# Optimization experiments

Hardware: AMD Instinct MI355X
Metric: run time of the kernel (lower is better)

The kernel has to match this reference:

```python
import jax, jax.numpy as jnp
import numpy as np

T = 2048
HID = 4096
H = 32
HKV = 8
D = 128
EPS = 1e-5
THETA = 1e6
WINDOW = 1024


def setup_inputs() -> dict:
    key = jax.random.key(0)
    k1, k2, k3 = jax.random.split(key, 3)
    return {
        "positions": jnp.arange(T, dtype=jnp.int32),
        "hidden_states": jax.random.normal(k1, (T, HID), dtype=jnp.float32),
        "w_qkv": jax.random.normal(k2, (HID, (H + 2 * HKV) * D), dtype=jnp.float32) * 0.02,
        "q_norm_w": jnp.ones((D,), dtype=jnp.float32),
        "k_norm_w": jnp.ones((D,), dtype=jnp.float32),
        "w_o": jax.random.normal(k3, (H * D, HID), dtype=jnp.float32) * 0.02,
    }


def _rmsnorm(x, w):
    # per-head RMSNorm over last dim (head_dim)
    var = jnp.mean(x * x, axis=-1, keepdims=True)
    return x * jax.lax.rsqrt(var + EPS) * w


def _rope_neox(x, positions):
    # x: [T, heads, D]; neox style: rotate halves
    half = D // 2
    inv_freq = 1.0 / (THETA ** (jnp.arange(0, half, dtype=jnp.float32) / half))
    ang = positions.astype(jnp.float32)[:, None] * inv_freq  # [T, half]
    cos = jnp.cos(ang)[:, None, :]
    sin = jnp.sin(ang)[:, None, :]
    x1, x2 = x[..., :half], x[..., half:]
    return jnp.concatenate([x1 * cos - x2 * sin, x2 * cos + x1 * sin], axis=-1)


def reference(positions, hidden_states, w_qkv, q_norm_w, k_norm_w, w_o):
    qkv = hidden_states @ w_qkv  # [T, (H+2Hkv)*D]
    q, k, v = jnp.split(qkv, [H * D, (H + HKV) * D], axis=-1)
    q = _rmsnorm(q.reshape(T, H, D), q_norm_w)
    k = _rmsnorm(k.reshape(T, HKV, D), k_norm_w)
    v = v.reshape(T, HKV, D)

    q = _rope_neox(q, positions)
    k = _rope_neox(k, positions)

    # GQA: expand kv heads to H
    rep = H // HKV
    k = jnp.repeat(k, rep, axis=1)  # [T, H, D]
    v = jnp.repeat(v, rep, axis=1)

    scale = D ** -0.5
    scores = jnp.einsum('thd,shd->hts', q, k) * scale  # [H, T, T]
    i = jnp.arange(T)[:, None]
    j = jnp.arange(T)[None, :]
    mask = (j <= i) & (i - j < WINDOW)  # causal + sliding window
    scores = jnp.where(mask[None], scores, -jnp.inf)
    probs = jax.nn.softmax(scores, axis=-1)
    attn = jnp.einsum('hts,shd->thd', probs, v).reshape(T, H * D)
    return attn @ w_o
```

## Files before the change

### kernel.cpp

```cpp
#include <hip/hip_runtime.h>
#include <hip/hip_bf16.h>
#include <stdint.h>

#define T_SEQ  2048
#define HIDDEN 4096
#define NHEAD  32
#define NKV    8
#define HDIM   128
#define NQKV   6144
#define WINDOW 1024
#define SCALE  0.08838834764831845f
#define SHIFT  12.0f

typedef __attribute__((ext_vector_type(8))) short          short8;
typedef __attribute__((ext_vector_type(8))) unsigned short ushort8_t;
typedef __attribute__((ext_vector_type(4))) float          floatx4;

__device__ __forceinline__ unsigned short f2bf(float f) {
    union { float f; unsigned int u; } v; v.f = f;
    unsigned int u = v.u;
    unsigned int r = (u + 0x7FFFu + ((u >> 16) & 1u)) >> 16;
    return (unsigned short)r;
}
__device__ __forceinline__ float bf2f(unsigned short u) {
    union { unsigned int u; float f; } v; v.u = ((unsigned int)u) << 16;
    return v.f;
}

#define GLOBAL_AS(p) ((const __attribute__((address_space(1))) void*)(p))
#define LDS_AS(p)    ((__attribute__((address_space(3))) void*)(p))

#define S_BARRIER() do { asm volatile("" ::: "memory");  \
                         __builtin_amdgcn_s_barrier();   \
                         asm volatile("" ::: "memory"); } while (0)

__global__ __launch_bounds__(256) void convert_bf16_kernel(
        const float* __restrict__ X, unsigned short* __restrict__ Y, int n4) {
    int i = blockIdx.x * blockDim.x + threadIdx.x;
    if (i < n4) {
        float4 v = ((const float4*)X)[i];
        ushort4 o;
        o.x = f2bf(v.x); o.y = f2bf(v.y); o.z = f2bf(v.z); o.w = f2bf(v.w);
        ((ushort4*)Y)[i] = o;
    }
}

__global__ __launch_bounds__(256) void transpose_bf16_kernel(
        const float* __restrict__ W, unsigned short* __restrict__ Wt, int K, int N) {
    __shared__ float tile[128][33];
    const int n0 = blockIdx.x * 32, k0 = blockIdx.y * 128;
    const int tid = threadIdx.x;
    const int rr = tid >> 3, cc = tid & 7;
    #pragma unroll
    for (int p = 0; p < 4; ++p) {
        int r = p * 32 + rr;
        float4 v = *(const float4*)&W[(size_t)(k0 + r) * N + n0 + cc * 4];
        tile[r][cc * 4 + 0] = v.x; tile[r][cc * 4 + 1] = v.y;
        tile[r][cc * 4 + 2] = v.z; tile[r][cc * 4 + 3] = v.w;
    }
    __syncthreads();
    const int nL = tid >> 3, kc = tid & 7;
    #pragma unroll
    for (int q = 0; q < 2; ++q) {
        int kbase = kc * 8 + q * 64;
        ushort8_t o;
        #pragma unroll
        for (int j = 0; j < 8; ++j) o[j] = f2bf(tile[kbase + j][nL]);
        *(ushort8_t*)&Wt[(size_t)(n0 + nL) * K + k0 + kbase] = o;
    }
}

#define STG3_A(bufi, kt, r)                                                       \
    __builtin_amdgcn_global_load_lds(                                             \
        GLOBAL_AS(A + (size_t)(m0 + rRow[r]) * K + ((kt) << 6) + rOff[r]),        \
        LDS_AS(&As3[bufi][((r) * 256 + tid) * 8]), 16, 0, 0)
#define STG3_B(bufi, kt, r)                                                       \
    __builtin_amdgcn_global_load_lds(                                             \
        GLOBAL_AS(B + (size_t)(n0 + rRow[r]) * K + ((kt) << 6) + rOff[r]),        \
        LDS_AS(&Bs3[bufi][((r) * 256 + tid) * 8]), 16, 0, 0)

template <bool BF16_OUT>
__global__ __launch_bounds__(256, 2) void gemm_bt3_kernel(
        const unsigned short* __restrict__ A,
        const unsigned short* __restrict__ B,
        void* __restrict__ Cv, int M, int N, int K) {
    __shared__ __align__(16) unsigned short As3[2][128 * 64];
    __shared__ __align__(16) unsigned short Bs3[2][128 * 64];

    const int tid  = threadIdx.x;
    const int lane = tid & 63, wave = tid >> 6;
    const int wr = wave >> 1, wc = wave & 1;
    const int lrow = lane & 15, hi = lane >> 4;

    const int nwg = gridDim.x * gridDim.y;
    int wg = blockIdx.y * gridDim.x + blockIdx.x;
    wg = (wg & 7) * (nwg >> 3) + (wg >> 3);
    const int bx = wg % gridDim.x;
    const int by = wg / gridDim.x;
    const int m0 = by * 128, n0 = bx * 128;

    const int NT = K >> 6;

    int rRow[4], rOff[4];
    #pragma unroll
    for (int r = 0; r < 4; ++r) {
        int idx = r * 256 + tid;
        int row = idx >> 3;
        rRow[r] = row;
        rOff[r] = ((idx & 7) ^ (row & 7)) * 8;
    }

    const int sA0   = (hi ^ (lrow & 7)) * 8;
    const int aBase = (wr * 64 + lrow) * 64;
    const int bBase = (wc * 64 + lrow) * 64;

    floatx4 acc[4][4] = {};

    auto kstep = [&](int cur, int t2, int mode) {
        const unsigned short* ap = &As3[cur][0];
        const unsigned short* bp = &Bs3[cur][0];
        short8 af[4][2], bf[4][2];
        #pragma unroll
        for (int m = 0; m < 4; ++m)
            #pragma unroll
            for (int kh = 0; kh < 2; ++kh)
                af[m][kh] = *(const short8*)(ap + aBase + m * 1024 + (sA0 ^ (kh << 5)));
        #pragma unroll
        for (int n = 0; n < 4; ++n)
            #pragma unroll
            for (int kh = 0; kh < 2; ++kh)
                bf[n][kh] = *(const short8*)(bp + bBase + n * 1024 + (sA0 ^ (kh << 5)));
        asm volatile("s_waitcnt lgkmcnt(0)" ::: "memory");
        __builtin_amdgcn_s_barrier();
        asm volatile("" ::: "memory");
        if (mode == 0) {
            #pragma unroll
            for (int r = 0; r < 4; ++r) STG3_A(cur, t2, r);
            #pragma unroll
            for (int r = 0; r < 4; ++r) STG3_B(cur, t2, r);
        }
        __builtin_amdgcn_s_setprio(1);
        #pragma unroll
        for (int m = 0; m < 4; ++m)
            #pragma unroll
            for (int n = 0; n < 4; ++n) {
                acc[m][n] = __builtin_amdgcn_mfma_f32_16x16x32_bf16(
                    af[m][0], bf[n][0], acc[m][n], 0, 0, 0);
                acc[m][n] = __builtin_amdgcn_mfma_f32_16x16x32_bf16(
                    af[m][1], bf[n][1], acc[m][n], 0, 0, 0);
            }
        __builtin_amdgcn_s_setprio(0);
        if (mode == 0) {
            asm volatile("s_waitcnt vmcnt(8)" ::: "memory");
            __builtin_amdgcn_s_barrier();
            asm volatile("" ::: "memory");
        } else if (mode == 1) {
            asm volatile("s_waitcnt vmcnt(0)" ::: "memory");
            __builtin_amdgcn_s_barrier();
            asm volatile("" ::: "memory");
        }
    };

    #pragma unroll
    for (int r = 0; r < 4; ++r) STG3_A(0, 0, r);
    #pragma unroll
    for (int r = 0; r < 4; ++r) STG3_B(0, 0, r);
    #pragma unroll
    for (int r = 0; r < 4; ++r) STG3_A(1, 1, r);
    #pragma unroll
    for (int r = 0; r < 4; ++r) STG3_B(1, 1, r);
    asm volatile("s_waitcnt vmcnt(8)" ::: "memory");
    S_BARRIER();

    int t = 0;
    for (; t < NT - 2; ++t) kstep(t & 1, t + 2, 0);
    kstep(t & 1, 0, 1); ++t;
    kstep(t & 1, 0, 2);

    const int rowb = hi * 4, col = lrow;
    #pragma unroll
    for (int mi = 0; mi < 4; ++mi)
        #pragma unroll
        for (int ni = 0; ni < 4; ++ni) {
            size_t base = (size_t)(m0 + wr * 64 + mi * 16 + rowb) * N
                        + (n0 + wc * 64 + ni * 16 + col);
            #pragma unroll
            for (int r = 0; r < 4; ++r) {
                if (BF16_OUT)
                    ((unsigned short*)Cv)[base + (size_t)r * N] = f2bf(acc[mi][ni][r]);
                else
                    ((float*)Cv)[base + (size_t)r * N] = acc[mi][ni][r];
            }
        }
}

#define STG4_A(bufi, kt, r)                                                       \
    __builtin_amdgcn_global_load_lds(                                             \
        GLOBAL_AS(A + (size_t)(m0 + rRowA[r]) * K + ((kt) << 6) + rOffA[r]),      \
        LDS_AS(&As4[bufi][((r) * 256 + tid) * 8]), 16, 0, 0)
#define STG4_B(bufi, kt, r)                                                       \
    __builtin_amdgcn_global_load_lds(                                             \
        GLOBAL_AS(B + (size_t)(n0 + rRowB[r]) * K + ((kt) << 6) + rOffB[r]),      \
        LDS_AS(&Bs4[bufi][((r) * 256 + tid) * 8]), 16, 0, 0)

template <bool BF16_OUT>
__global__ __launch_bounds__(256, 2) void gemm_bt4_kernel(
        const unsigned short* __restrict__ A,
        const unsigned short* __restrict__ B,
        void* __restrict__ Cv, int M, int N, int K) {
    __shared__ __align__(16) unsigned short As4[2][128 * 64];
    __shared__ __align__(16) unsigned short Bs4[2][192 * 64];

    const int tid  = threadIdx.x;
    const int lane = tid & 63, wave = tid >> 6;
    const int wr = wave >> 1, wc = wave & 1;
    const int lrow = lane & 15, hi = lane >> 4;

    const int nwg = gridDim.x * gridDim.y;
    int wg = blockIdx.y * gridDim.x + blockIdx.x;
    wg = (wg & 7) * (nwg >> 3) + (wg >> 3);
    const int by = wg % gridDim.x;
    const int bx = wg / gridDim.x;
    const int m0 = by * 128, n0 = bx * 192;

    const int NT = K >> 6;

    int rRowA[4], rOffA[4];
    #pragma unroll
    for (int r = 0; r < 4; ++r) {
        int idx = r * 256 + tid;
        int row = idx >> 3;
        rRowA[r] = row;
        rOffA[r] = ((idx & 7) ^ (row & 7)) * 8;
    }
    int rRowB[6], rOffB[6];
    #pragma unroll
    for (int r = 0; r < 6; ++r) {
        int idx = r * 256 + tid;
        int row = idx >> 3;
        rRowB[r] = row;
        rOffB[r] = ((idx & 7) ^ (row & 7)) * 8;
    }

    const int sA0   = (hi ^ (lrow & 7)) * 8;
    const int aBase = (wr * 64 + lrow) * 64;
    const int bBase = (wc * 96 + lrow) * 64;

    floatx4 acc[4][6] = {};

    auto kstep = [&](int cur, int t2, int mode) {
        const unsigned short* ap = &As4[cur][0];
        const unsigned short* bp = &Bs4[cur][0];
        short8 af[4][2], bf[6][2];
        #pragma unroll
        for (int m = 0; m < 4; ++m)
            #pragma unroll
            for (int kh = 0; kh < 2; ++kh)
                af[m][kh] = *(const short8*)(ap + aBase + m * 1024 + (sA0 ^ (kh << 5)));
        #pragma unroll
        for (int n = 0; n < 6; ++n)
            #pragma unroll
            for (int kh = 0; kh < 2; ++kh)
                bf[n][kh] = *(const short8*)(bp + bBase + n * 1024 + (sA0 ^ (kh << 5)));
        asm volatile("s_waitcnt lgkmcnt(0)" ::: "memory");
        __builtin_amdgcn_s_barrier();
        asm volatile("" ::: "memory");
        if (mode == 0) {
            #pragma unroll
            for (int r = 0; r < 4; ++r) STG4_A(cur, t2, r);
            #pragma unroll
            for (int r = 0; r < 6; ++r) STG4_B(cur, t2, r);
        }
        __builtin_amdgcn_s_setprio(1);
        #pragma unroll
        for (int m = 0; m < 4; ++m)
            #pragma unroll
            for (int n = 0; n < 6; ++n) {
                acc[m][n] = __builtin_amdgcn_mfma_f32_16x16x32_bf16(
                    af[m][0], bf[n][0], acc[m][n], 0, 0, 0);
                acc[m][n] = __builtin_amdgcn_mfma_f32_16x16x32_bf16(
                    af[m][1], bf[n][1], acc[m][n], 0, 0, 0);
            }
        __builtin_amdgcn_s_setprio(0);
        if (mode == 0) {
            asm volatile("s_waitcnt vmcnt(10)" ::: "memory");
            __builtin_amdgcn_s_barrier();
            asm volatile("" ::: "memory");
        } else if (mode == 1) {
            asm volatile("s_waitcnt vmcnt(0)" ::: "memory");
            __builtin_amdgcn_s_barrier();
            asm volatile("" ::: "memory");
        }
    };

    #pragma unroll
    for (int r = 0; r < 4; ++r) STG4_A(0, 0, r);
    #pragma unroll
    for (int r = 0; r < 6; ++r) STG4_B(0, 0, r);
    #pragma unroll
    for (int r = 0; r < 4; ++r) STG4_A(1, 1, r);
    #pragma unroll
    for (int r = 0; r < 6; ++r) STG4_B(1, 1, r);
    asm volatile("s_waitcnt vmcnt(10)" ::: "memory");
    S_BARRIER();

    int t = 0;
    for (; t < NT - 2; ++t) kstep(t & 1, t + 2, 0);
    kstep(t & 1, 0, 1); ++t;
    kstep(t & 1, 0, 2);

    const int rowb = hi * 4, col = lrow;
    #pragma unroll
    for (int mi = 0; mi < 4; ++mi)
        #pragma unroll
        for (int ni = 0; ni < 6; ++ni) {
            size_t base = (size_t)(m0 + wr * 64 + mi * 16 + rowb) * N
                        + (n0 + wc * 96 + ni * 16 + col);
            #pragma unroll
            for (int r = 0; r < 4; ++r) {
                if (BF16_OUT)
                    ((unsigned short*)Cv)[base + (size_t)r * N] = f2bf(acc[mi][ni][r]);
                else
                    ((float*)Cv)[base + (size_t)r * N] = acc[mi][ni][r];
            }
        }
}

__global__ __launch_bounds__(256) void rope_table_kernel(
        const int* __restrict__ positions, float2* __restrict__ rope) {
    int idx = blockIdx.x * 256 + threadIdx.x;
    int t = idx >> 6, i = idx & 63;
    float inv_freq = expf((float)i * -0.2158673524681918f);
    float sn, cs;
    sincosf((float)positions[t] * inv_freq, &sn, &cs);
    rope[idx] = make_float2(cs, sn);
}

__global__ __launch_bounds__(256) void qkv_post_kernel(
        const unsigned short* __restrict__ qkv, const float2* __restrict__ rope,
        const float* __restrict__ qw, const float* __restrict__ kw,
        unsigned short* __restrict__ qb,
        unsigned short* __restrict__ kb,
        unsigned short* __restrict__ vbT) {
    const int head = blockIdx.y;
    const int t0   = blockIdx.x * 32;
    const int tid  = threadIdx.x;

    if (head < 40) {
        const int r  = tid >> 3;
        const int q8 = tid & 7;
        const int t  = t0 + r;
        const unsigned short* src = qkv + (size_t)t * NQKV
                         + (head < 32 ? head * 128 : 4096 + (head - 32) * 128)
                         + q8 * 16;
        const float* w = (head < 32) ? qw : kw;

        ushort8_t u0 = *(const ushort8_t*)src;
        ushort8_t u1 = *(const ushort8_t*)(src + 8);
        float x[16];
        #pragma unroll
        for (int j = 0; j < 8; ++j) { x[j] = bf2f(u0[j]); x[8 + j] = bf2f(u1[j]); }

        float ss = 0.f;
        #pragma unroll
        for (int j = 0; j < 16; ++j) ss = fmaf(x[j], x[j], ss);
        ss += __shfl_xor(ss, 1); ss += __shfl_xor(ss, 2); ss += __shfl_xor(ss, 4);
        float sc = rsqrtf(ss * (1.f / 128.f) + 1e-5f);

        float xn[16], xp[16];
        #pragma unroll
        for (int j = 0; j < 16; ++j) xn[j] = x[j] * sc * w[q8 * 16 + j];
        #pragma unroll
        for (int j = 0; j < 16; ++j) xp[j] = __shfl_xor(xn[j], 4);

        const float2* rp = rope + (size_t)t * 64 + (q8 & 3) * 16;
        ushort8_t o0, o1;
        #pragma unroll
        for (int j = 0; j < 8; ++j) {
            float2 cs = rp[j];
            float res = (q8 < 4) ? (xn[j] * cs.x - xp[j] * cs.y)
                                 : (xn[j] * cs.x + xp[j] * cs.y);
            o0[j] = f2bf(res);
        }
        #pragma unroll
        for (int j = 0; j < 8; ++j) {
            float2 cs = rp[8 + j];
            float res = (q8 < 4) ? (xn[8+j] * cs.x - xp[8+j] * cs.y)
                                 : (xn[8+j] * cs.x + xp[8+j] * cs.y);
            o1[j] = f2bf(res);
        }
        unsigned short* dst = (head < 32)
            ? qb + ((size_t)t * 32 + head) * 128 + q8 * 16
            : kb + ((size_t)t * 8 + (head - 32)) * 128 + q8 * 16;
        *(ushort8_t*)dst       = o0;
        *(ushort8_t*)(dst + 8) = o1;
    } else {
        __shared__ float tile[128][33];
        const int hk = head - 40;
        {
            const int r = tid >> 3, c8 = tid & 7;
            const unsigned short* src =
                qkv + (size_t)(t0 + r) * NQKV + 5120 + hk * 128 + c8 * 16;
            ushort8_t u0 = *(const ushort8_t*)src;
            ushort8_t u1 = *(const ushort8_t*)(src + 8);
            #pragma unroll
            for (int j = 0; j < 8; ++j) {
                tile[c8 * 16 + j][r]     = bf2f(u0[j]);
                tile[c8 * 16 + 8 + j][r] = bf2f(u1[j]);
            }
        }
        __syncthreads();
        {
            const int d = tid >> 1, th = tid & 1;
            ushort8_t o0, o1;
            #pragma unroll
            for (int j = 0; j < 8; ++j) o0[j] = f2bf(tile[d][th * 16 + j]);
            #pragma unroll
            for (int j = 0; j < 8; ++j) o1[j] = f2bf(tile[d][th * 16 + 8 + j]);
            unsigned short* dst = vbT + ((size_t)hk * 128 + d) * T_SEQ + t0 + th * 16;
            *(ushort8_t*)dst       = o0;
            *(ushort8_t*)(dst + 8) = o1;
        }
    }
}

__global__ __launch_bounds__(256) void attention_kernel(
        const unsigned short* __restrict__ qb,
        const unsigned short* __restrict__ kb,
        const unsigned short* __restrict__ vbT,
        unsigned short* __restrict__ attnb) {
    const int h    = blockIdx.x & 31;
    const int Q0   = (blockIdx.x >> 5) * 64;
    const int tid  = threadIdx.x, wave = tid >> 6, lane = tid & 63;
    const int keyA = lane & 15, g = lane >> 4;
    const int hk   = h >> 2;
    const int qlo  = Q0 + wave * 16;

    __shared__ __align__(16) unsigned short ks [2][32 * 128];
    __shared__ __align__(16) unsigned short vsT[2][128 * 32];
    __shared__ __align__(16) unsigned short Pa [4 * 16 * 40];

    unsigned short* pw = Pa + wave * 640;

    int kRow[2], kOff[2], vD[2], vOff[2];
    #pragma unroll
    for (int i = 0; i < 2; ++i) {
        int c = i * 256 + tid;
        {   int row = c >> 4, u = c & 15;
            kRow[i] = row; kOff[i] = (u ^ (row & 7)) * 8; }
        {   int d = c >> 2, u = c & 3;
            vD[i] = d; vOff[i] = (u ^ (d & 3)) * 8; }
    }

    auto stage = [&](int buf, int s0) {
        #pragma unroll
        for (int i = 0; i < 2; ++i) {
            int c = i * 256 + tid;
            const unsigned short* kp =
                kb + ((size_t)(s0 + kRow[i]) * 8 + hk) * 128 + kOff[i];
            __builtin_amdgcn_global_load_lds(GLOBAL_AS(kp),
                LDS_AS(&ks[buf][c * 8]), 16, 0, 0);
            const unsigned short* vp =
                vbT + ((size_t)hk * 128 + vD[i]) * T_SEQ + s0 + vOff[i];
            __builtin_amdgcn_global_load_lds(GLOBAL_AS(vp),
                LDS_AS(&vsT[buf][c * 8]), 16, 0, 0);
        }
    };

    short8 qa[4];
    {
        const unsigned short* qp = qb + ((size_t)(qlo + keyA) * 32 + h) * 128 + g * 8;
        #pragma unroll
        for (int s = 0; s < 4; ++s) qa[s] = *(const short8*)(qp + s * 32);
    }

    floatx4 acc[8] = {};
    float l_part[4] = {0.f, 0.f, 0.f, 0.f};

    const int s_begin = (Q0 >= WINDOW) ? ((Q0 - (WINDOW - 1)) & ~31) : 0;
    const int s_end   = Q0 + 63;

    stage(0, s_begin);
    asm volatile("s_waitcnt vmcnt(0)" ::: "memory");
    S_BARRIER();

    int cur = 0;
    for (int s0 = s_begin; s0 <= s_end; s0 += 32) {
        if (s0 + 32 <= s_end) stage(cur ^ 1, s0 + 32);

        if (s0 <= qlo + 15 && s0 + 31 >= qlo - (WINDOW - 1)) {
            const unsigned short* ksb  = &ks[cur][0];
            const unsigned short* vsb  = &vsT[cur][0];
            floatx4 sa0 = {}, sa1 = {};
            #pragma unroll
            for (int kst = 0; kst < 4; ++kst) {
                int u = g + 4 * kst;
                short8 k0 = *(const short8*)(ksb + keyA * 128 + (u ^ (keyA & 7)) * 8);
                short8 k1 = *(const short8*)(ksb + (16 + keyA) * 128 + (u ^ ((16 + keyA) & 7)) * 8);
                sa0 = __builtin_amdgcn_mfma_f32_16x16x32_bf16(qa[kst], k0, sa0, 0, 0, 0);
                sa1 = __builtin_amdgcn_mfma_f32_16x16x32_bf16(qa[kst], k1, sa1, 0, 0, 0);
            }
            float p0[4], p1[4];
            #pragma unroll
            for (int r = 0; r < 4; ++r) {
                int row = qlo + 4 * g + r;
                int sA = s0 + keyA, sB = sA + 16;
                bool vA = (sA <= row) && (row - sA < WINDOW);
                bool vB = (sB <= row) && (row - sB < WINDOW);
                p0[r] = vA ? __expf(fmaf(sa0[r], SCALE, -SHIFT)) : 0.f;
                p1[r] = vB ? __expf(fmaf(sa1[r], SCALE, -SHIFT)) : 0.f;
                l_part[r] += p0[r] + p1[r];
            }
            #pragma unroll
            for (int r = 0; r < 4; ++r) {
                pw[(4 * g + r) * 40 + keyA]      = f2bf(p0[r]);
                pw[(4 * g + r) * 40 + keyA + 16] = f2bf(p1[r]);
            }
            short8 pf = *(const short8*)(pw + keyA * 40 + g * 8);

            #pragma unroll
            for (int t = 0; t < 8; ++t) {
                int d = t * 16 + keyA;
                short8 vf = *(const short8*)(vsb + d * 32 + (g ^ (d & 3)) * 8);
                acc[t] = __builtin_amdgcn_mfma_f32_16x16x32_bf16(pf, vf, acc[t], 0, 0, 0);
            }
        }
        asm volatile("s_waitcnt vmcnt(0)" ::: "memory");
        S_BARRIER();
        cur ^= 1;
    }

    float inv[4];
    #pragma unroll
    for (int r = 0; r < 4; ++r) {
        float l = l_part[r];
        l += __shfl_xor(l, 1); l += __shfl_xor(l, 2);
        l += __shfl_xor(l, 4); l += __shfl_xor(l, 8);
        inv[r] = 1.f / l;
    }
    #pragma unroll
    for (int t = 0; t < 8; ++t)
        #pragma unroll
        for (int r = 0; r < 4; ++r)
            attnb[(size_t)(qlo + 4 * g + r) * 4096 + h * 128 + t * 16 + keyA] =
                f2bf(acc[t][r] * inv[r]);
}

extern "C" void kernel_launch(void* const* d_in, const int* in_sizes, int n_in,
                              void* d_out, int out_size, void* d_ws, size_t ws_size,
                              hipStream_t stream) {
    const int*   positions = (const int*)  d_in[0];
    const float* hs        = (const float*)d_in[1];
    const float* w_qkv     = (const float*)d_in[2];
    const float* q_norm_w  = (const float*)d_in[3];
    const float* k_norm_w  = (const float*)d_in[4];
    const float* w_o       = (const float*)d_in[5];
    float* out = (float*)d_out;

    char* ws = (char*)d_ws;
    unsigned short* hsb   = (unsigned short*)(ws);
    unsigned short* wqkvt = (unsigned short*)(ws + (size_t)(16u << 20));
    unsigned short* wot   = (unsigned short*)(ws + (size_t)(64u << 20));
    unsigned short* qkvb  = (unsigned short*)(ws + (size_t)(96u << 20));
    unsigned short* qb    = (unsigned short*)(ws + (size_t)(16u << 20));
    unsigned short* kb    = (unsigned short*)(ws + (size_t)(32u << 20));
    unsigned short* vbT   = (unsigned short*)(ws + (size_t)(36u << 20));
    float2*         rope  = (float2*)        (ws + (size_t)(40u << 20));
    unsigned short* attnb = hsb;

    convert_bf16_kernel<<<dim3((T_SEQ * HIDDEN / 4 + 255) / 256), 256, 0, stream>>>(
        hs, hsb, T_SEQ * HIDDEN / 4);
    transpose_bf16_kernel<<<dim3(NQKV / 32, HIDDEN / 128), 256, 0, stream>>>(
        w_qkv, wqkvt, HIDDEN, NQKV);
    transpose_bf16_kernel<<<dim3(HIDDEN / 32, HIDDEN / 128), 256, 0, stream>>>(
        w_o, wot, HIDDEN, HIDDEN);
    gemm_bt4_kernel<true><<<dim3(T_SEQ / 128, NQKV / 192), 256, 0, stream>>>(
        hsb, wqkvt, qkvb, T_SEQ, NQKV, HIDDEN);
    rope_table_kernel<<<dim3(T_SEQ * 64 / 256), 256, 0, stream>>>(positions, rope);
    qkv_post_kernel<<<dim3(T_SEQ / 32, 48), 256, 0, stream>>>(
        qkvb, rope, q_norm_w, k_norm_w, qb, kb, vbT);
    attention_kernel<<<dim3((T_SEQ / 64) * NHEAD), 256, 0, stream>>>(
        qb, kb, vbT, attnb);
    gemm_bt3_kernel<false><<<dim3(HIDDEN / 128, T_SEQ / 128), 256, 0, stream>>>(
        attnb, wot, out, T_SEQ, HIDDEN, HIDDEN);
}
```

Measured before the change: 488.1 us.

## Triple-buffer output-projection GEMM with 256x128 tiles and 512 threads

Converts the output-projection GEMM from a double-buffered 128x128 tile with 256 threads to a triple-buffered 256x128 tile with 512 threads (8 waves). Global-to-LDS prefetch for step t+2 is now issued at the start of each k-step into the third buffer. This removes the mid-step barrier and lgkmcnt wait that guarded buffer reuse. The grid shrinks to 256 workgroups, one per CU, and LDS use rises to about 144KB per block, which lowers occupancy and may leave fewer blocks to hide latency.

```diff
diff --git a/kernel.cpp b/kernel.cpp
--- a/kernel.cpp
+++ b/kernel.cpp
@@ -72,20 +72,20 @@
 
 #define STG3_A(bufi, kt, r)                                                       \
     __builtin_amdgcn_global_load_lds(                                             \
-        GLOBAL_AS(A + (size_t)(m0 + rRow[r]) * K + ((kt) << 6) + rOff[r]),        \
-        LDS_AS(&As3[bufi][((r) * 256 + tid) * 8]), 16, 0, 0)
+        GLOBAL_AS(A + (size_t)(m0 + rRowA[r]) * K + ((kt) << 6) + rOffA[r]),      \
+        LDS_AS(&As3[bufi][((r) * 512 + tid) * 8]), 16, 0, 0)
 #define STG3_B(bufi, kt, r)                                                       \
     __builtin_amdgcn_global_load_lds(                                             \
-        GLOBAL_AS(B + (size_t)(n0 + rRow[r]) * K + ((kt) << 6) + rOff[r]),        \
-        LDS_AS(&Bs3[bufi][((r) * 256 + tid) * 8]), 16, 0, 0)
+        GLOBAL_AS(B + (size_t)(n0 + rRowB[r]) * K + ((kt) << 6) + rOffB[r]),      \
+        LDS_AS(&Bs3[bufi][((r) * 512 + tid) * 8]), 16, 0, 0)
 
 template <bool BF16_OUT>
-__global__ __launch_bounds__(256, 2) void gemm_bt3_kernel(
+__global__ __launch_bounds__(512, 1) void gemm_bt3_kernel(
         const unsigned short* __restrict__ A,
         const unsigned short* __restrict__ B,
         void* __restrict__ Cv, int M, int N, int K) {
-    __shared__ __align__(16) unsigned short As3[2][128 * 64];
-    __shared__ __align__(16) unsigned short Bs3[2][128 * 64];
+    __shared__ __align__(16) unsigned short As3[3][256 * 64];
+    __shared__ __align__(16) unsigned short Bs3[3][128 * 64];
 
     const int tid  = threadIdx.x;
     const int lane = tid & 63, wave = tid >> 6;
@@ -97,17 +97,25 @@
     wg = (wg & 7) * (nwg >> 3) + (wg >> 3);
     const int bx = wg % gridDim.x;
     const int by = wg / gridDim.x;
-    const int m0 = by * 128, n0 = bx * 128;
+    const int m0 = by * 256, n0 = bx * 128;
 
     const int NT = K >> 6;
 
-    int rRow[4], rOff[4];
+    int rRowA[4], rOffA[4];
     #pragma unroll
     for (int r = 0; r < 4; ++r) {
-        int idx = r * 256 + tid;
+        int idx = r * 512 + tid;
         int row = idx >> 3;
-        rRow[r] = row;
-        rOff[r] = ((idx & 7) ^ (row & 7)) * 8;
+        rRowA[r] = row;
+        rOffA[r] = ((idx & 7) ^ (row & 7)) * 8;
+    }
+    int rRowB[2], rOffB[2];
+    #pragma unroll
+    for (int r = 0; r < 2; ++r) {
+        int idx = r * 512 + tid;
+        int row = idx >> 3;
+        rRowB[r] = row;
+        rOffB[r] = ((idx & 7) ^ (row & 7)) * 8;
     }
 
     const int sA0   = (hi ^ (lrow & 7)) * 8;
@@ -117,6 +125,13 @@
     floatx4 acc[4][4] = {};
 
     auto kstep = [&](int cur, int t2, int mode) {
+        if (mode == 0) {
+            int stg = cur + 2; if (stg >= 3) stg -= 3;
+            #pragma unroll
+            for (int r = 0; r < 4; ++r) STG3_A(stg, t2, r);
+            #pragma unroll
+            for (int r = 0; r < 2; ++r) STG3_B(stg, t2, r);
+        }
         const unsigned short* ap = &As3[cur][0];
         const unsigned short* bp = &Bs3[cur][0];
         short8 af[4][2], bf[4][2];
@@ -130,15 +145,6 @@
             #pragma unroll
             for (int kh = 0; kh < 2; ++kh)
                 bf[n][kh] = *(const short8*)(bp + bBase + n * 1024 + (sA0 ^ (kh << 5)));
-        asm volatile("s_waitcnt lgkmcnt(0)" ::: "memory");
-        __builtin_amdgcn_s_barrier();
-        asm volatile("" ::: "memory");
-        if (mode == 0) {
-            #pragma unroll
-            for (int r = 0; r < 4; ++r) STG3_A(cur, t2, r);
-            #pragma unroll
-            for (int r = 0; r < 4; ++r) STG3_B(cur, t2, r);
-        }
         __builtin_amdgcn_s_setprio(1);
         #pragma unroll
         for (int m = 0; m < 4; ++m)
@@ -151,7 +157,7 @@
             }
         __builtin_amdgcn_s_setprio(0);
         if (mode == 0) {
-            asm volatile("s_waitcnt vmcnt(8)" ::: "memory");
+            asm volatile("s_waitcnt vmcnt(6)" ::: "memory");
             __builtin_amdgcn_s_barrier();
             asm volatile("" ::: "memory");
         } else if (mode == 1) {
@@ -164,18 +170,23 @@
     #pragma unroll
     for (int r = 0; r < 4; ++r) STG3_A(0, 0, r);
     #pragma unroll
-    for (int r = 0; r < 4; ++r) STG3_B(0, 0, r);
+    for (int r = 0; r < 2; ++r) STG3_B(0, 0, r);
     #pragma unroll
     for (int r = 0; r < 4; ++r) STG3_A(1, 1, r);
     #pragma unroll
-    for (int r = 0; r < 4; ++r) STG3_B(1, 1, r);
-    asm volatile("s_waitcnt vmcnt(8)" ::: "memory");
+    for (int r = 0; r < 2; ++r) STG3_B(1, 1, r);
+    asm volatile("s_waitcnt vmcnt(6)" ::: "memory");
     S_BARRIER();
 
+    int cur = 0;
     int t = 0;
-    for (; t < NT - 2; ++t) kstep(t & 1, t + 2, 0);
-    kstep(t & 1, 0, 1); ++t;
-    kstep(t & 1, 0, 2);
+    for (; t < NT - 2; ++t) {
+        kstep(cur, t + 2, 0);
+        cur = (cur == 2) ? 0 : cur + 1;
+    }
+    kstep(cur, 0, 1);
+    cur = (cur == 2) ? 0 : cur + 1;
+    kstep(cur, 0, 2);
 
     const int rowb = hi * 4, col = lrow;
     #pragma unroll
@@ -581,6 +592,6 @@
         qkvb, rope, q_norm_w, k_norm_w, qb, kb, vbT);
     attention_kernel<<<dim3((T_SEQ / 64) * NHEAD), 256, 0, stream>>>(
         qb, kb, vbT, attnb);
-    gemm_bt3_kernel<false><<<dim3(HIDDEN / 128, T_SEQ / 128), 256, 0, stream>>>(
+    gemm_bt3_kernel<false><<<dim3(HIDDEN / 128, T_SEQ / 256), 512, 0, stream>>>(
         attnb, wot, out, T_SEQ, HIDDEN, HIDDEN);
 }
```

Result: slower. 519.9 us (+6.5%).
